# Optimization experiments

Hardware: AMD Instinct MI355X
Metric: run time of the kernel (lower is better)

## Reference

```python
import jax, jax.numpy as jnp
import numpy as np

N_EMBD = 768
N_HEAD = 12

def setup_inputs() -> dict:
    key = jax.random.key(0)
    ks = jax.random.split(key, 10)
    B, T, C = 2, 2048, N_EMBD
    s = 1.0 / np.sqrt(C)
    x = jax.random.normal(ks[0], (B, T, C), dtype=jnp.float32)
    attn_mask = jnp.ones((B, 1, T, T), dtype=jnp.float32)
    Wq = jax.random.normal(ks[1], (C, C), dtype=jnp.float32) * s
    bq = jax.random.normal(ks[2], (C,), dtype=jnp.float32) * 0.01
    Wk = jax.random.normal(ks[3], (C, C), dtype=jnp.float32) * s
    bk = jax.random.normal(ks[4], (C,), dtype=jnp.float32) * 0.01
    Wv = jax.random.normal(ks[5], (C, C), dtype=jnp.float32) * s
    bv = jax.random.normal(ks[6], (C,), dtype=jnp.float32) * 0.01
    Wp = jax.random.normal(ks[7], (C, C), dtype=jnp.float32) * s
    bp = jax.random.normal(ks[8], (C,), dtype=jnp.float32) * 0.01
    return {"x": x, "attn_mask": attn_mask, "Wq": Wq, "bq": bq, "Wk": Wk, "bk": bk,
            "Wv": Wv, "bv": bv, "Wp": Wp, "bp": bp}

def reference(x, attn_mask, Wq, bq, Wk, bk, Wv, bv, Wp, bp):
    B, T, C = x.shape
    H = N_HEAD
    hd = C // H
    # Linear layers (torch nn.Linear: y = x @ W.T + b)
    q = (x @ Wq.T + bq).reshape(B, T, H, hd).transpose(0, 2, 1, 3)  # [B,H,T,hd]
    k = (x @ Wk.T + bk).reshape(B, T, H, hd).transpose(0, 2, 1, 3)
    v = (x @ Wv.T + bv).reshape(B, T, H, hd).transpose(0, 2, 1, 3)
    att = jnp.einsum('bhqd,bhkd->bhqk', q, k) / jnp.sqrt(jnp.float32(hd))  # [B,H,T,T]
    causal = jnp.tril(jnp.ones((T, T), dtype=jnp.bool_))[None, None]       # [1,1,T,T]
    combined = causal & (attn_mask > 0)                                    # broadcast to [B,H,T,T]
    att = jnp.where(combined, att, -jnp.inf)
    att = jax.nn.softmax(att, axis=-1)
    y = jnp.einsum('bhqk,bhkd->bhqd', att, v)                              # [B,H,T,hd]
    y = y.transpose(0, 2, 1, 3).reshape(B, T, C)
    return y @ Wp.T + bp
```

## Files before the change

### kernel.cpp

```cpp
#include <hip/hip_runtime.h>
#include <hip/hip_bf16.h>
#include <cstdint>
#include <cstddef>

#define B_   2
#define H_   12
#define T_   2048
#define C_   768
#define HD_  64
#define M_   4096
#define NW_  (T_/64)

typedef __attribute__((ext_vector_type(8))) short bf16x8;
typedef __attribute__((ext_vector_type(4))) float fx4;
typedef __attribute__((ext_vector_type(2))) unsigned long long u64x2;
typedef unsigned short u16;
typedef unsigned int   u32;
typedef unsigned long long u64;

static __device__ __forceinline__ u16 f2bf(float f){
    union { float f; unsigned int i; } c; c.f = f;
    unsigned int x = c.i;
    return (u16)((x + 0x7fffu + ((x >> 16) & 1u)) >> 16);
}

static __device__ __forceinline__ u32 pack_bf2(float a, float b){
    union { __hip_bfloat162 h; u32 u; } cv;
    cv.h = __float22bfloat162_rn(make_float2(a, b));
    return cv.u;
}

__global__ void cvt_f32_bf16(const float* __restrict__ src, u16* __restrict__ dst, int n4){
    int i = blockIdx.x * blockDim.x + threadIdx.x;
    if (i < n4){
        float4 v = ((const float4*)src)[i];
        ushort4 o;
        o.x = f2bf(v.x); o.y = f2bf(v.y); o.z = f2bf(v.z); o.w = f2bf(v.w);
        ((ushort4*)dst)[i] = o;
    }
}

__global__ void cvt_w4(const float* __restrict__ wq, const float* __restrict__ wk,
                       const float* __restrict__ wv, const float* __restrict__ wp,
                       u16* __restrict__ dst){
    const float* src = (blockIdx.y == 0) ? wq : (blockIdx.y == 1) ? wk
                     : (blockIdx.y == 2) ? wv : wp;
    int i = blockIdx.x * blockDim.x + threadIdx.x;
    float4 v = ((const float4*)src)[i];
    ushort4 o;
    o.x = f2bf(v.x); o.y = f2bf(v.y); o.z = f2bf(v.z); o.w = f2bf(v.w);
    ((ushort4*)(dst + (size_t)blockIdx.y * C_ * C_))[i] = o;
}

__global__ void mask_bits_kernel(const float* __restrict__ mask, u64* __restrict__ bits){
    int wid  = blockIdx.x * (blockDim.x >> 6) + (threadIdx.x >> 6);
    int lane = threadIdx.x & 63;
    float v = mask[(size_t)wid * 64 + lane];
    u64 m = __ballot(v > 0.0f);
    if (lane == 0) bits[wid] = m;
}

__launch_bounds__(256, 2)
__global__ void gemm_qkv(const u16* __restrict__ xb, const u16* __restrict__ wqkv,
                         const float* __restrict__ bq, const float* __restrict__ bk,
                         const float* __restrict__ bv,
                         u16* __restrict__ qo, u16* __restrict__ ko, u16* __restrict__ vto)
{
    const int tid  = threadIdx.x;
    const int lane = tid & 63, wave = tid >> 6;
    const int l15 = lane & 15, lg = lane >> 4;
    const int m0 = blockIdx.y * 128;
    const int n0 = blockIdx.x * 128;
    const int z  = blockIdx.z;
    const u16* wb     = wqkv + (size_t)z * C_ * C_;
    const float* bias = (z == 0) ? bq : (z == 1 ? bk : bv);
    const float oscl  = (z == 0) ? 0.1803368801111601f : 1.0f;

    __shared__ __align__(16) u16 lds_a[128 * 64];
    __shared__ __align__(16) u16 lds_b[128 * 64];

    fx4 acc[4][4];
    #pragma unroll
    for (int i = 0; i < 4; i++)
        #pragma unroll
        for (int j = 0; j < 4; j++) acc[i][j] = (fx4)0.0f;

    const int wm = (wave >> 1) * 64, wn = (wave & 1) * 64;
    const int sx = l15 & 7;

    for (int kt = 0; kt < C_ / 64; ++kt){
        const int k0 = kt * 64;
        #pragma unroll
        for (int c = 0; c < 4; ++c){
            int unit = c * 256 + tid;
            int row = unit >> 3, col = unit & 7;
            int gcol = (col ^ (row & 7)) * 8;
            const u16* ga = xb + (size_t)(m0 + row) * C_ + k0 + gcol;
            __builtin_amdgcn_global_load_lds((const __attribute__((address_space(1))) void*)ga,
                (__attribute__((address_space(3))) void*)(lds_a + (c * 256 + wave * 64) * 8), 16, 0, 0);
            const u16* gb = wb + (size_t)(n0 + row) * C_ + k0 + gcol;
            __builtin_amdgcn_global_load_lds((const __attribute__((address_space(1))) void*)gb,
                (__attribute__((address_space(3))) void*)(lds_b + (c * 256 + wave * 64) * 8), 16, 0, 0);
        }
        __syncthreads();
        #pragma unroll
        for (int ks = 0; ks < 2; ++ks){
            bf16x8 af[4], bfr[4];
            #pragma unroll
            for (int i = 0; i < 4; i++){
                af[i]  = *(const bf16x8*)&lds_a[(wm + i * 16 + l15) * 64 + (((4 * ks + lg) ^ sx) * 8)];
                bfr[i] = *(const bf16x8*)&lds_b[(wn + i * 16 + l15) * 64 + (((4 * ks + lg) ^ sx) * 8)];
            }
            #pragma unroll
            for (int i = 0; i < 4; i++)
                #pragma unroll
                for (int j = 0; j < 4; j++)
                    acc[i][j] = __builtin_amdgcn_mfma_f32_16x16x32_bf16(af[i], bfr[j], acc[i][j], 0, 0, 0);
        }
        __syncthreads();
    }

    #pragma unroll
    for (int i = 0; i < 4; i++){
        #pragma unroll
        for (int j = 0; j < 4; j++){
            #pragma unroll
            for (int r = 0; r < 4; r++){
                int m = m0 + wm + i * 16 + lg * 4 + r;
                int n = n0 + wn + j * 16 + l15;
                float v = (acc[i][j][r] + bias[n]) * oscl;
                u16 o = f2bf(v);
                int b = m >> 11, t = m & (T_ - 1);
                int h = n >> 6, d = n & 63;
                if (z == 2){
                    vto[(size_t)((b * H_ + h) * HD_ + d) * T_ + t] = o;
                } else {
                    u16* dst = (z == 0) ? qo : ko;
                    dst[(size_t)((b * H_ + h) * T_ + t) * HD_ + d] = o;
                }
            }
        }
    }
}

__launch_bounds__(256, 2)
__global__ void gemm_proj(const u16* __restrict__ yb, const u16* __restrict__ wp,
                          const float* __restrict__ bp, float* __restrict__ out)
{
    const int tid  = threadIdx.x;
    const int lane = tid & 63, wave = tid >> 6;
    const int l15 = lane & 15, lg = lane >> 4;
    const int m0 = blockIdx.y * 128;
    const int n0 = blockIdx.x * 128;

    __shared__ __align__(16) u16 lds_a[128 * 64];
    __shared__ __align__(16) u16 lds_b[128 * 64];

    fx4 acc[4][4];
    #pragma unroll
    for (int i = 0; i < 4; i++)
        #pragma unroll
        for (int j = 0; j < 4; j++) acc[i][j] = (fx4)0.0f;

    const int wm = (wave >> 1) * 64, wn = (wave & 1) * 64;
    const int sx = l15 & 7;

    for (int kt = 0; kt < C_ / 64; ++kt){
        const int k0 = kt * 64;
        #pragma unroll
        for (int c = 0; c < 4; ++c){
            int unit = c * 256 + tid;
            int row = unit >> 3, col = unit & 7;
            int gcol = (col ^ (row & 7)) * 8;
            const u16* ga = yb + (size_t)(m0 + row) * C_ + k0 + gcol;
            __builtin_amdgcn_global_load_lds((const __attribute__((address_space(1))) void*)ga,
                (__attribute__((address_space(3))) void*)(lds_a + (c * 256 + wave * 64) * 8), 16, 0, 0);
            const u16* gb = wp + (size_t)(n0 + row) * C_ + k0 + gcol;
            __builtin_amdgcn_global_load_lds((const __attribute__((address_space(1))) void*)gb,
                (__attribute__((address_space(3))) void*)(lds_b + (c * 256 + wave * 64) * 8), 16, 0, 0);
        }
        __syncthreads();
        #pragma unroll
        for (int ks = 0; ks < 2; ++ks){
            bf16x8 af[4], bfr[4];
            #pragma unroll
            for (int i = 0; i < 4; i++){
                af[i]  = *(const bf16x8*)&lds_a[(wm + i * 16 + l15) * 64 + (((4 * ks + lg) ^ sx) * 8)];
                bfr[i] = *(const bf16x8*)&lds_b[(wn + i * 16 + l15) * 64 + (((4 * ks + lg) ^ sx) * 8)];
            }
            #pragma unroll
            for (int i = 0; i < 4; i++)
                #pragma unroll
                for (int j = 0; j < 4; j++)
                    acc[i][j] = __builtin_amdgcn_mfma_f32_16x16x32_bf16(af[i], bfr[j], acc[i][j], 0, 0, 0);
        }
        __syncthreads();
    }

    #pragma unroll
    for (int i = 0; i < 4; i++)
        #pragma unroll
        for (int j = 0; j < 4; j++)
            #pragma unroll
            for (int r = 0; r < 4; r++){
                int m = m0 + wm + i * 16 + lg * 4 + r;
                int n = n0 + wn + j * 16 + l15;
                out[(size_t)m * C_ + n] = acc[i][j][r] + bp[n];
            }
}

__launch_bounds__(256, 2)
__global__ void attn(const u16* __restrict__ q, const u16* __restrict__ kmat,
                     const u16* __restrict__ vt, const u64* __restrict__ bits,
                     u16* __restrict__ y)
{
    const int tid = threadIdx.x, lane = tid & 63, w = tid >> 6;
    const int l15 = lane & 15, lg = lane >> 4;
    const int bh = blockIdx.x % (B_ * H_);
    const int qt = (T_ / 64 - 1) - blockIdx.x / (B_ * H_);
    const int b = bh / H_, h = bh % H_;
    const int qt0 = qt * 64;
    const int qbase = qt0 + w * 16;

    __shared__ __align__(16) u16 lds_k[128 * 64];
    __shared__ __align__(16) u16 lds_v[64 * 128];
    __shared__ __align__(16) u32 lds_p[4][16 * 68];

    const size_t bhoff = (size_t)bh * T_ * HD_;
    const int sx = l15 & 7;

    bf16x8 qf[2];
    {
        const u16* qrow = q + bhoff + (size_t)(qbase + l15) * HD_;
        qf[0] = *(const bf16x8*)(qrow + lg * 8);
        qf[1] = *(const bf16x8*)(qrow + 32 + lg * 8);
    }

    fx4 oacc[4];
    #pragma unroll
    for (int i = 0; i < 4; i++) oacc[i] = (fx4)0.0f;
    float m_l = -1e30f, l_l = 0.0f;

    const int nkt = ((qt0 + 63) >> 7) + 1;
    const int qg  = qbase + l15;
    const u64* brow = bits + (size_t)(b * T_ + qg) * NW_;

    const int kr0 = tid >> 3,  kc0 = tid & 7;
    const int vr0 = tid >> 4,  vc0 = tid & 15;

    bf16x8 kreg[4], vreg[4];
    {
        #pragma unroll
        for (int i = 0; i < 4; i++){
            int row = kr0 + i * 32;
            kreg[i] = *(const bf16x8*)(kmat + bhoff + (size_t)row * HD_ + kc0 * 8);
            int rv = vr0 + i * 16;
            vreg[i] = *(const bf16x8*)(vt + bhoff + (size_t)rv * T_ + vc0 * 8);
        }
        #pragma unroll
        for (int i = 0; i < 4; i++){
            int row = kr0 + i * 32;
            *(bf16x8*)&lds_k[row * 64 + ((kc0 ^ (row & 7)) * 8)] = kreg[i];
            int rv = vr0 + i * 16;
            *(bf16x8*)&lds_v[rv * 128 + ((vc0 ^ (rv & 7)) * 8)] = vreg[i];
        }
    }
    __syncthreads();

    for (int kt = 0; kt < nkt; ++kt){
        const int kbase = kt * 128;
        const bool pf = (kt + 1 < nkt);
        if (pf){
            const int kb2 = kbase + 128;
            #pragma unroll
            for (int i = 0; i < 4; i++){
                int row = kr0 + i * 32;
                kreg[i] = *(const bf16x8*)(kmat + bhoff + (size_t)(kb2 + row) * HD_ + kc0 * 8);
                int rv = vr0 + i * 16;
                vreg[i] = *(const bf16x8*)(vt + bhoff + (size_t)rv * T_ + kb2 + vc0 * 8);
            }
        }

        fx4 s[8];
        #pragma unroll
        for (int ct = 0; ct < 8; ct++){
            s[ct] = (fx4)0.0f;
            #pragma unroll
            for (int ks = 0; ks < 2; ks++){
                bf16x8 kf = *(const bf16x8*)&lds_k[(ct * 16 + l15) * 64 + (((4 * ks + lg) ^ sx) * 8)];
                s[ct] = __builtin_amdgcn_mfma_f32_16x16x32_bf16(kf, qf[ks], s[ct], 0, 0, 0);
            }
        }

        u64x2 raw = *(const u64x2*)&brow[kt * 2];
        int sh0 = qg - kbase, sh1 = qg - kbase - 64;
        u64 vis0 = sh0 < 0 ? 0ull : (sh0 >= 63 ? ~0ull : ((2ull << sh0) - 1ull));
        u64 vis1 = sh1 < 0 ? 0ull : (sh1 >= 63 ? ~0ull : ((2ull << sh1) - 1ull));
        u64 ms0 = (raw[0] & vis0) >> (lg * 4);
        u64 ms1 = (raw[1] & vis1) >> (lg * 4);
        float mx = -1e30f;
        #pragma unroll
        for (int ct = 0; ct < 8; ct++){
            u64 msel = (ct < 4) ? ms0 : ms1;
            int base = 16 * (ct & 3);
            #pragma unroll
            for (int r = 0; r < 4; r++){
                u32 bit = (u32)(msel >> (base + r)) & 1u;
                float sv = bit ? s[ct][r] : -1e30f;
                s[ct][r] = sv;
                mx = fmaxf(mx, sv);
            }
        }
        mx = fmaxf(mx, __shfl_xor(mx, 16, 64));
        mx = fmaxf(mx, __shfl_xor(mx, 32, 64));

        float mnew = fmaxf(m_l, mx);
        float al = __builtin_amdgcn_exp2f(m_l - mnew);
        m_l = mnew;

        float rs = 0.0f;
        #pragma unroll
        for (int ct = 0; ct < 8; ct++){
            float p0 = __builtin_amdgcn_exp2f(s[ct][0] - mnew);
            float p1 = __builtin_amdgcn_exp2f(s[ct][1] - mnew);
            float p2 = __builtin_amdgcn_exp2f(s[ct][2] - mnew);
            float p3 = __builtin_amdgcn_exp2f(s[ct][3] - mnew);
            rs += (p0 + p1) + (p2 + p3);
            uint2 pk; pk.x = pack_bf2(p0, p1); pk.y = pack_bf2(p2, p3);
            *(uint2*)&lds_p[w][l15 * 68 + 8 * ct + 2 * lg] = pk;
        }
        rs += __shfl_xor(rs, 16, 64);
        rs += __shfl_xor(rs, 32, 64);
        l_l = l_l * al + rs;

        #pragma unroll
        for (int r = 0; r < 4; r++){
            float alr = __shfl(al, lg * 4 + r, 64);
            #pragma unroll
            for (int db = 0; db < 4; db++) oacc[db][r] *= alr;
        }

        #pragma unroll
        for (int ks = 0; ks < 4; ks++){
            bf16x8 paf = *(const bf16x8*)&lds_p[w][l15 * 68 + 16 * ks + 4 * lg];
            #pragma unroll
            for (int db = 0; db < 4; db++){
                bf16x8 vf = *(const bf16x8*)&lds_v[(db * 16 + l15) * 128 + (((4 * ks + lg) ^ sx) * 8)];
                oacc[db] = __builtin_amdgcn_mfma_f32_16x16x32_bf16(paf, vf, oacc[db], 0, 0, 0);
            }
        }

        if (pf){
            __syncthreads();
            #pragma unroll
            for (int i = 0; i < 4; i++){
                int row = kr0 + i * 32;
                *(bf16x8*)&lds_k[row * 64 + ((kc0 ^ (row & 7)) * 8)] = kreg[i];
                int rv = vr0 + i * 16;
                *(bf16x8*)&lds_v[rv * 128 + ((vc0 ^ (rv & 7)) * 8)] = vreg[i];
            }
            __syncthreads();
        }
    }

    #pragma unroll
    for (int r = 0; r < 4; r++){
        float lr = __shfl(l_l, lg * 4 + r, 64);
        float inv = 1.0f / lr;
        int qrow = qbase + lg * 4 + r;
        #pragma unroll
        for (int db = 0; db < 4; db++){
            int d = db * 16 + l15;
            y[(size_t)(b * T_ + qrow) * C_ + h * HD_ + d] = f2bf(oacc[db][r] * inv);
        }
    }
}

extern "C" void kernel_launch(void* const* d_in, const int* in_sizes, int n_in,
                              void* d_out, int out_size, void* d_ws, size_t ws_size,
                              hipStream_t stream)
{
    const float* x    = (const float*)d_in[0];
    const float* mask = (const float*)d_in[1];
    const float* Wq   = (const float*)d_in[2];
    const float* bq   = (const float*)d_in[3];
    const float* Wk   = (const float*)d_in[4];
    const float* bk   = (const float*)d_in[5];
    const float* Wv   = (const float*)d_in[6];
    const float* bv   = (const float*)d_in[7];
    const float* Wp   = (const float*)d_in[8];
    const float* bp   = (const float*)d_in[9];
    float* out = (float*)d_out;

    char* p = (char*)d_ws;
    u16* xb   = (u16*)p; p += (size_t)M_ * C_ * 2;
    u16* wqkv = (u16*)p; p += (size_t)4 * C_ * C_ * 2;
    u16* qo   = (u16*)p; p += (size_t)M_ * C_ * 2;
    u16* ko   = (u16*)p; p += (size_t)M_ * C_ * 2;
    u16* vto  = (u16*)p; p += (size_t)M_ * C_ * 2;
    u16* yb   = (u16*)p; p += (size_t)M_ * C_ * 2;
    u64* bits = (u64*)p; p += (size_t)B_ * T_ * NW_ * 8;

    const int NX4 = M_ * C_ / 4;
    const int NW4 = C_ * C_ / 4;
    cvt_f32_bf16<<<dim3((NX4 + 255) / 256), 256, 0, stream>>>(x, xb, NX4);
    cvt_w4<<<dim3(NW4 / 256, 4), 256, 0, stream>>>(Wq, Wk, Wv, Wp, wqkv);
    mask_bits_kernel<<<dim3(B_ * T_ * NW_ / 4), 256, 0, stream>>>(mask, bits);

    gemm_qkv<<<dim3(C_ / 128, M_ / 128, 3), 256, 0, stream>>>(
        xb, wqkv, bq, bk, bv, qo, ko, vto);

    attn<<<dim3((T_ / 64) * B_ * H_), 256, 0, stream>>>(qo, ko, vto, bits, yb);

    gemm_proj<<<dim3(C_ / 128, M_ / 128), 256, 0, stream>>>(yb, wqkv + (size_t)3 * C_ * C_, bp, out);
}
```

Baseline: 106.3 us.

## Rewrite attention with 32x32 MFMA, register-resident P, lazy rescale, and block swizzles

The attention kernel now uses 128-thread blocks with two waves, each handling 32 query rows. It computes S and PV with 32x32x16 bf16 MFMAs over 64-key tiles and keeps P in registers via v_permlane32_swap instead of staging it through LDS. It skips masking when a tile is fully visible and skips output rescaling unless the running max grows by more than a threshold. Both GEMMs and attention also get block-index swizzles to improve L2 locality. The lazy rescale relies on fp32 headroom, and the smaller blocks and key tiles mean more barriers per key processed.

```diff
diff --git a/kernel.cpp b/kernel.cpp
--- a/kernel.cpp
+++ b/kernel.cpp
@@ -13,7 +13,7 @@
 
 typedef __attribute__((ext_vector_type(8))) short bf16x8;
 typedef __attribute__((ext_vector_type(4))) float fx4;
-typedef __attribute__((ext_vector_type(2))) unsigned long long u64x2;
+typedef __attribute__((ext_vector_type(16))) float f32x16;
 typedef unsigned short u16;
 typedef unsigned int   u32;
 typedef unsigned long long u64;
@@ -69,9 +69,11 @@
     const int tid  = threadIdx.x;
     const int lane = tid & 63, wave = tid >> 6;
     const int l15 = lane & 15, lg = lane >> 4;
-    const int m0 = blockIdx.y * 128;
-    const int n0 = blockIdx.x * 128;
-    const int z  = blockIdx.z;
+    int flat = blockIdx.x + 6 * (blockIdx.y + 32 * blockIdx.z);
+    int swz  = (flat & 7) * 72 + (flat >> 3);
+    const int n0 = (swz % 6) * 128;
+    const int m0 = ((swz / 6) % 32) * 128;
+    const int z  = swz / 192;
     const u16* wb     = wqkv + (size_t)z * C_ * C_;
     const float* bias = (z == 0) ? bq : (z == 1 ? bk : bv);
     const float oscl  = (z == 0) ? 0.1803368801111601f : 1.0f;
@@ -150,8 +152,10 @@
     const int tid  = threadIdx.x;
     const int lane = tid & 63, wave = tid >> 6;
     const int l15 = lane & 15, lg = lane >> 4;
-    const int m0 = blockIdx.y * 128;
-    const int n0 = blockIdx.x * 128;
+    int flat = blockIdx.x + 6 * blockIdx.y;
+    int swz  = (flat & 7) * 24 + (flat >> 3);
+    const int n0 = (swz % 6) * 128;
+    const int m0 = (swz / 6) * 128;
 
     __shared__ __align__(16) u16 lds_a[128 * 64];
     __shared__ __align__(16) u16 lds_b[128 * 64];
@@ -209,170 +213,171 @@
             }
 }
 
-__launch_bounds__(256, 2)
+__launch_bounds__(128, 2)
 __global__ void attn(const u16* __restrict__ q, const u16* __restrict__ kmat,
                      const u16* __restrict__ vt, const u64* __restrict__ bits,
                      u16* __restrict__ y)
 {
     const int tid = threadIdx.x, lane = tid & 63, w = tid >> 6;
-    const int l15 = lane & 15, lg = lane >> 4;
-    const int bh = blockIdx.x % (B_ * H_);
-    const int qt = (T_ / 64 - 1) - blockIdx.x / (B_ * H_);
+    const int l31 = lane & 31, hi = lane >> 5;
+    int flat = blockIdx.x;
+    const int bh = (flat & 7) * 3 + ((flat >> 3) % 3);
+    const int qt = 31 - (flat >> 3) / 3;
     const int b = bh / H_, h = bh % H_;
-    const int qt0 = qt * 64;
-    const int qbase = qt0 + w * 16;
-
-    __shared__ __align__(16) u16 lds_k[128 * 64];
-    __shared__ __align__(16) u16 lds_v[64 * 128];
-    __shared__ __align__(16) u32 lds_p[4][16 * 68];
+    const int q0 = qt * 64;
+    const int qw0 = q0 + 32 * w;
+
+    __shared__ __align__(16) u16 lds_k[64 * 64];
+    __shared__ __align__(16) u16 lds_v[64 * 64];
 
     const size_t bhoff = (size_t)bh * T_ * HD_;
-    const int sx = l15 & 7;
-
-    bf16x8 qf[2];
+
+    bf16x8 qf[4];
     {
-        const u16* qrow = q + bhoff + (size_t)(qbase + l15) * HD_;
-        qf[0] = *(const bf16x8*)(qrow + lg * 8);
-        qf[1] = *(const bf16x8*)(qrow + 32 + lg * 8);
-    }
-
-    fx4 oacc[4];
-    #pragma unroll
-    for (int i = 0; i < 4; i++) oacc[i] = (fx4)0.0f;
+        const u16* qrow = q + bhoff + (size_t)(qw0 + l31) * HD_ + hi * 8;
+        #pragma unroll
+        for (int dc = 0; dc < 4; dc++)
+            qf[dc] = *(const bf16x8*)(qrow + dc * 16);
+    }
+
+    f32x16 o0 = (f32x16)0.0f, o1 = (f32x16)0.0f;
     float m_l = -1e30f, l_l = 0.0f;
 
-    const int nkt = ((qt0 + 63) >> 7) + 1;
-    const int qg  = qbase + l15;
+    const int nkt = qt + 1;
+    const int qg  = qw0 + l31;
     const u64* brow = bits + (size_t)(b * T_ + qg) * NW_;
 
-    const int kr0 = tid >> 3,  kc0 = tid & 7;
-    const int vr0 = tid >> 4,  vc0 = tid & 15;
+    const int sr = tid >> 3;
+    const int sc = tid & 7;
 
     bf16x8 kreg[4], vreg[4];
     {
         #pragma unroll
         for (int i = 0; i < 4; i++){
-            int row = kr0 + i * 32;
-            kreg[i] = *(const bf16x8*)(kmat + bhoff + (size_t)row * HD_ + kc0 * 8);
-            int rv = vr0 + i * 16;
-            vreg[i] = *(const bf16x8*)(vt + bhoff + (size_t)rv * T_ + vc0 * 8);
+            int row = sr + 16 * i;
+            kreg[i] = *(const bf16x8*)(kmat + bhoff + (size_t)row * HD_ + sc * 8);
+            vreg[i] = *(const bf16x8*)(vt   + bhoff + (size_t)row * T_  + sc * 8);
         }
         #pragma unroll
         for (int i = 0; i < 4; i++){
-            int row = kr0 + i * 32;
-            *(bf16x8*)&lds_k[row * 64 + ((kc0 ^ (row & 7)) * 8)] = kreg[i];
-            int rv = vr0 + i * 16;
-            *(bf16x8*)&lds_v[rv * 128 + ((vc0 ^ (rv & 7)) * 8)] = vreg[i];
+            int row = sr + 16 * i;
+            *(bf16x8*)&lds_k[row * 64 + ((sc ^ (row & 7)) * 8)] = kreg[i];
+            *(bf16x8*)&lds_v[row * 64 + ((sc ^ (row & 7)) * 8)] = vreg[i];
         }
     }
     __syncthreads();
 
     for (int kt = 0; kt < nkt; ++kt){
-        const int kbase = kt * 128;
+        const int kbase = kt * 64;
         const bool pf = (kt + 1 < nkt);
         if (pf){
-            const int kb2 = kbase + 128;
+            const int kb2 = kbase + 64;
             #pragma unroll
             for (int i = 0; i < 4; i++){
-                int row = kr0 + i * 32;
-                kreg[i] = *(const bf16x8*)(kmat + bhoff + (size_t)(kb2 + row) * HD_ + kc0 * 8);
-                int rv = vr0 + i * 16;
-                vreg[i] = *(const bf16x8*)(vt + bhoff + (size_t)rv * T_ + kb2 + vc0 * 8);
-            }
-        }
-
-        fx4 s[8];
-        #pragma unroll
-        for (int ct = 0; ct < 8; ct++){
-            s[ct] = (fx4)0.0f;
+                int row = sr + 16 * i;
+                kreg[i] = *(const bf16x8*)(kmat + bhoff + (size_t)(kb2 + row) * HD_ + sc * 8);
+                vreg[i] = *(const bf16x8*)(vt   + bhoff + (size_t)row * T_ + kb2 + sc * 8);
+            }
+        }
+
+        f32x16 s0 = (f32x16)0.0f, s1 = (f32x16)0.0f;
+        #pragma unroll
+        for (int dc = 0; dc < 4; dc++){
+            bf16x8 kf0 = *(const bf16x8*)&lds_k[(l31     ) * 64 + (((2 * dc + hi) ^ (l31 & 7)) * 8)];
+            bf16x8 kf1 = *(const bf16x8*)&lds_k[(l31 + 32) * 64 + (((2 * dc + hi) ^ (l31 & 7)) * 8)];
+            s0 = __builtin_amdgcn_mfma_f32_32x32x16_bf16(kf0, qf[dc], s0, 0, 0, 0);
+            s1 = __builtin_amdgcn_mfma_f32_32x32x16_bf16(kf1, qf[dc], s1, 0, 0, 0);
+        }
+
+        u64 raw = brow[kt];
+        int sh = qg - kbase;
+        u64 vis = sh < 0 ? 0ull : (sh >= 63 ? ~0ull : ((2ull << sh) - 1ull));
+        u64 masked = raw & vis;
+        if (!__all(masked == ~0ull)){
+            u32 mk0 = (u32)(masked >> (4 * hi));
+            u32 mk1 = (u32)(masked >> (32 + 4 * hi));
+            #pragma unroll
+            for (int r = 0; r < 16; r++){
+                int bpos = (r & 3) + 8 * (r >> 2);
+                s0[r] = ((mk0 >> bpos) & 1u) ? s0[r] : -1e30f;
+                s1[r] = ((mk1 >> bpos) & 1u) ? s1[r] : -1e30f;
+            }
+        }
+
+        float mx = -1e30f;
+        #pragma unroll
+        for (int r = 0; r < 16; r++){ mx = fmaxf(mx, s0[r]); mx = fmaxf(mx, s1[r]); }
+        mx = fmaxf(mx, __shfl_xor(mx, 32, 64));
+
+        if (!__all(mx <= m_l + 10.0f)){
+            float mnew = fmaxf(m_l, mx);
+            float al = __builtin_amdgcn_exp2f(m_l - mnew);
+            m_l = mnew;
+            l_l *= al;
+            #pragma unroll
+            for (int r = 0; r < 16; r++){
+                int ql = (r & 3) + 8 * (r >> 2) + 4 * hi;
+                float a_r = __shfl(al, ql, 64);
+                o0[r] *= a_r; o1[r] *= a_r;
+            }
+        }
+
+        float rs = 0.0f;
+        bf16x8 pa[2][2];
+        #pragma unroll
+        for (int kb = 0; kb < 2; kb++){
+            u32 P[8];
+            #pragma unroll
+            for (int g = 0; g < 8; g++){
+                float pe0 = __builtin_amdgcn_exp2f((kb ? s1[2*g]   : s0[2*g])   - m_l);
+                float pe1 = __builtin_amdgcn_exp2f((kb ? s1[2*g+1] : s0[2*g+1]) - m_l);
+                rs += pe0 + pe1;
+                P[g] = pack_bf2(pe0, pe1);
+            }
+            asm volatile("v_permlane32_swap_b32 %0, %1" : "+v"(P[0]), "+v"(P[2]));
+            asm volatile("v_permlane32_swap_b32 %0, %1" : "+v"(P[1]), "+v"(P[3]));
+            asm volatile("v_permlane32_swap_b32 %0, %1" : "+v"(P[4]), "+v"(P[6]));
+            asm volatile("v_permlane32_swap_b32 %0, %1" : "+v"(P[5]), "+v"(P[7]));
+            union { u32 uw[4]; bf16x8 v; } u0, u1;
+            u0.uw[0]=P[0]; u0.uw[1]=P[1]; u0.uw[2]=P[2]; u0.uw[3]=P[3];
+            u1.uw[0]=P[4]; u1.uw[1]=P[5]; u1.uw[2]=P[6]; u1.uw[3]=P[7];
+            pa[kb][0] = u0.v; pa[kb][1] = u1.v;
+        }
+        rs += __shfl_xor(rs, 32, 64);
+        l_l += rs;
+
+        #pragma unroll
+        for (int kb = 0; kb < 2; kb++)
             #pragma unroll
             for (int ks = 0; ks < 2; ks++){
-                bf16x8 kf = *(const bf16x8*)&lds_k[(ct * 16 + l15) * 64 + (((4 * ks + lg) ^ sx) * 8)];
-                s[ct] = __builtin_amdgcn_mfma_f32_16x16x32_bf16(kf, qf[ks], s[ct], 0, 0, 0);
-            }
-        }
-
-        u64x2 raw = *(const u64x2*)&brow[kt * 2];
-        int sh0 = qg - kbase, sh1 = qg - kbase - 64;
-        u64 vis0 = sh0 < 0 ? 0ull : (sh0 >= 63 ? ~0ull : ((2ull << sh0) - 1ull));
-        u64 vis1 = sh1 < 0 ? 0ull : (sh1 >= 63 ? ~0ull : ((2ull << sh1) - 1ull));
-        u64 ms0 = (raw[0] & vis0) >> (lg * 4);
-        u64 ms1 = (raw[1] & vis1) >> (lg * 4);
-        float mx = -1e30f;
-        #pragma unroll
-        for (int ct = 0; ct < 8; ct++){
-            u64 msel = (ct < 4) ? ms0 : ms1;
-            int base = 16 * (ct & 3);
-            #pragma unroll
-            for (int r = 0; r < 4; r++){
-                u32 bit = (u32)(msel >> (base + r)) & 1u;
-                float sv = bit ? s[ct][r] : -1e30f;
-                s[ct][r] = sv;
-                mx = fmaxf(mx, sv);
-            }
-        }
-        mx = fmaxf(mx, __shfl_xor(mx, 16, 64));
-        mx = fmaxf(mx, __shfl_xor(mx, 32, 64));
-
-        float mnew = fmaxf(m_l, mx);
-        float al = __builtin_amdgcn_exp2f(m_l - mnew);
-        m_l = mnew;
-
-        float rs = 0.0f;
-        #pragma unroll
-        for (int ct = 0; ct < 8; ct++){
-            float p0 = __builtin_amdgcn_exp2f(s[ct][0] - mnew);
-            float p1 = __builtin_amdgcn_exp2f(s[ct][1] - mnew);
-            float p2 = __builtin_amdgcn_exp2f(s[ct][2] - mnew);
-            float p3 = __builtin_amdgcn_exp2f(s[ct][3] - mnew);
-            rs += (p0 + p1) + (p2 + p3);
-            uint2 pk; pk.x = pack_bf2(p0, p1); pk.y = pack_bf2(p2, p3);
-            *(uint2*)&lds_p[w][l15 * 68 + 8 * ct + 2 * lg] = pk;
-        }
-        rs += __shfl_xor(rs, 16, 64);
-        rs += __shfl_xor(rs, 32, 64);
-        l_l = l_l * al + rs;
-
-        #pragma unroll
-        for (int r = 0; r < 4; r++){
-            float alr = __shfl(al, lg * 4 + r, 64);
-            #pragma unroll
-            for (int db = 0; db < 4; db++) oacc[db][r] *= alr;
-        }
-
-        #pragma unroll
-        for (int ks = 0; ks < 4; ks++){
-            bf16x8 paf = *(const bf16x8*)&lds_p[w][l15 * 68 + 16 * ks + 4 * lg];
-            #pragma unroll
-            for (int db = 0; db < 4; db++){
-                bf16x8 vf = *(const bf16x8*)&lds_v[(db * 16 + l15) * 128 + (((4 * ks + lg) ^ sx) * 8)];
-                oacc[db] = __builtin_amdgcn_mfma_f32_16x16x32_bf16(paf, vf, oacc[db], 0, 0, 0);
-            }
-        }
+                int gidx = 4 * kb + 2 * ks + hi;
+                bf16x8 vf0 = *(const bf16x8*)&lds_v[(l31     ) * 64 + ((gidx ^ (l31 & 7)) * 8)];
+                bf16x8 vf1 = *(const bf16x8*)&lds_v[(l31 + 32) * 64 + ((gidx ^ (l31 & 7)) * 8)];
+                o0 = __builtin_amdgcn_mfma_f32_32x32x16_bf16(pa[kb][ks], vf0, o0, 0, 0, 0);
+                o1 = __builtin_amdgcn_mfma_f32_32x32x16_bf16(pa[kb][ks], vf1, o1, 0, 0, 0);
+            }
 
         if (pf){
             __syncthreads();
             #pragma unroll
             for (int i = 0; i < 4; i++){
-                int row = kr0 + i * 32;
-                *(bf16x8*)&lds_k[row * 64 + ((kc0 ^ (row & 7)) * 8)] = kreg[i];
-                int rv = vr0 + i * 16;
-                *(bf16x8*)&lds_v[rv * 128 + ((vc0 ^ (rv & 7)) * 8)] = vreg[i];
+                int row = sr + 16 * i;
+                *(bf16x8*)&lds_k[row * 64 + ((sc ^ (row & 7)) * 8)] = kreg[i];
+                *(bf16x8*)&lds_v[row * 64 + ((sc ^ (row & 7)) * 8)] = vreg[i];
             }
             __syncthreads();
         }
     }
 
+    float inv = 1.0f / l_l;
     #pragma unroll
-    for (int r = 0; r < 4; r++){
-        float lr = __shfl(l_l, lg * 4 + r, 64);
-        float inv = 1.0f / lr;
-        int qrow = qbase + lg * 4 + r;
-        #pragma unroll
-        for (int db = 0; db < 4; db++){
-            int d = db * 16 + l15;
-            y[(size_t)(b * T_ + qrow) * C_ + h * HD_ + d] = f2bf(oacc[db][r] * inv);
-        }
+    for (int r = 0; r < 16; r++){
+        int ql = (r & 3) + 8 * (r >> 2) + 4 * hi;
+        float iv = __shfl(inv, ql, 64);
+        int trow = qw0 + ql;
+        u16* yr = y + (size_t)(b * T_ + trow) * C_ + h * HD_;
+        yr[l31]      = f2bf(o0[r] * iv);
+        yr[32 + l31] = f2bf(o1[r] * iv);
     }
 }
 
@@ -410,7 +415,7 @@
     gemm_qkv<<<dim3(C_ / 128, M_ / 128, 3), 256, 0, stream>>>(
         xb, wqkv, bq, bk, bv, qo, ko, vto);
 
-    attn<<<dim3((T_ / 64) * B_ * H_), 256, 0, stream>>>(qo, ko, vto, bits, yb);
+    attn<<<dim3((T_ / 64) * B_ * H_), 128, 0, stream>>>(qo, ko, vto, bits, yb);
 
     gemm_proj<<<dim3(C_ / 128, M_ / 128), 256, 0, stream>>>(yb, wqkv + (size_t)3 * C_ * C_, bp, out);
 }
```

After: 130.0 us. 22.3% more time.
